# Performance work log

Hardware: AMD Instinct MI355X
Metric: run time of the kernel (lower is better)

The kernel has to match this reference:

```python
import jax, jax.numpy as jnp
import numpy as np
from jax import lax

DIM = 256
NUM_HEADS = 8
SPLIT = 7
IDX = 0  # vertical split: h_sp=h, w_sp=split_size
HEAD_DIM = DIM // NUM_HEADS
SCALE = HEAD_DIM ** -0.5


def setup_inputs() -> dict:
    key = jax.random.key(0)
    k1, k2, k3 = jax.random.split(key, 3)
    b, h, w = 16, 56, 56
    n = h * w
    qkv = jax.random.normal(k1, (3, b, n, DIM), dtype=jnp.float32)
    conv_w = jax.random.normal(k2, (DIM, 1, 3, 3), dtype=jnp.float32) * 0.1
    conv_b = jax.random.normal(k3, (DIM,), dtype=jnp.float32) * 0.1
    return {"qkv": qkv, "conv_w": conv_w, "conv_b": conv_b, "h": h, "w": w}


def _to_windows_heads(x, b, c, h, w, h_sp, w_sp):
    # (b, n, c) -> (b*nWin, num_heads, h_sp*w_sp, head_dim)
    x = x.transpose(0, 2, 1).reshape(b, c, h, w)
    x = x.reshape(b, c, h // h_sp, h_sp, w // w_sp, w_sp)
    x = x.transpose(0, 2, 4, 3, 5, 1).reshape(-1, h_sp * w_sp, c)
    return x.reshape(-1, h_sp * w_sp, NUM_HEADS, HEAD_DIM).transpose(0, 2, 1, 3)


def reference(qkv, conv_w, conv_b, h, w):
    q, k, v = qkv[0], qkv[1], qkv[2]
    b, n, c = q.shape
    h_sp, w_sp = (h, SPLIT) if IDX == 0 else (SPLIT, w)

    qw = _to_windows_heads(q, b, c, h, w, h_sp, w_sp) * SCALE
    kw = _to_windows_heads(k, b, c, h, w, h_sp, w_sp)

    # v as window images (b*nWin, c, h_sp, w_sp) for depthwise-conv LePE
    vimg = v.transpose(0, 2, 1).reshape(b, c, h, w)
    vimg = vimg.reshape(b, c, h // h_sp, h_sp, w // w_sp, w_sp)
    vimg = vimg.transpose(0, 2, 4, 1, 3, 5).reshape(-1, c, h_sp, w_sp)

    lepe = lax.conv_general_dilated(
        vimg, conv_w, window_strides=(1, 1), padding='SAME',
        dimension_numbers=('NCHW', 'OIHW', 'NCHW'), feature_group_count=c)
    lepe = lepe + conv_b[None, :, None, None]

    def _heads(t):  # (b', c, h_sp, w_sp) -> (b', heads, hw, head_dim)
        return t.reshape(-1, NUM_HEADS, HEAD_DIM, h_sp * w_sp).transpose(0, 1, 3, 2)

    vw = _heads(vimg)
    lepe = _heads(lepe)

    attn = jax.nn.softmax(jnp.einsum('whqd,whkd->whqk', qw, kw), axis=-1)
    x = jnp.einsum('whqk,whkd->whqd', attn, vw) + lepe  # (b', heads, hw, hd)

    x = x.transpose(0, 2, 1, 3).reshape(-1, h_sp * w_sp, c)
    # windows2img
    x = x.reshape(b, h // h_sp, w // w_sp, h_sp, w_sp, c)
    x = x.transpose(0, 1, 3, 2, 4, 5).reshape(b, h, w, c)
    return x.reshape(b, n, c)
```

## Files before the change

### kernel.cpp

```cpp
#include <hip/hip_runtime.h>
#include <math.h>


#define BATCH 16
#define HH 56
#define WW 56
#define WSP 7
#define NHEAD 8
#define HD 32
#define DIMC 256
#define NTOK 3136
#define S 392
#define SPAD 416
#define NCH 13
#define QT 25
#define QSCALE 0.17677669529663687f

typedef __attribute__((ext_vector_type(8))) short short8;
typedef __attribute__((ext_vector_type(4))) float f32x4;

#define MFMA(A, B, C) __builtin_amdgcn_mfma_f32_16x16x32_bf16((A), (B), (C), 0, 0, 0)

__device__ inline ushort bf16_rne(float f) {
    uint u = __float_as_uint(f);
    return (ushort)((u + 0x7FFFu + ((u >> 16) & 1u)) >> 16);
}
__device__ inline float bf16_f32(ushort h) { return __uint_as_float(((uint)h) << 16); }

__global__ __launch_bounds__(512, 1)
void lepe_attn_mfma(const float* __restrict__ qkv,
                    const float* __restrict__ conv_w,
                    const float* __restrict__ conv_b,
                    float* __restrict__ out)
{
    __shared__ ushort Kh_s[SPAD * HD];
    __shared__ ushort Kl_s[SPAD * HD];
    __shared__ ushort Vh_s[HD * SPAD];
    __shared__ ushort Vl_s[HD * SPAD];
    __shared__ ushort lepe_s[S * HD];
    __shared__ ushort P_s[8][2][16 * 40];

    const int tid  = threadIdx.x;
    const int lane = tid & 63;
    const int wv   = tid >> 6;
    const int ql   = lane & 15;
    const int g    = lane >> 4;
    const int slot = ((g ^ ((ql >> 1) & 3)) << 3);
    const int bid  = blockIdx.x;
    const int head = bid & 7;
    const int gw   = bid >> 3;
    const int b    = gw >> 3;
    const int wi   = gw & 7;
    const int coff = head * HD;

    const float* qbase = qkv + (size_t)b * NTOK * DIMC;
    const float* kbase = qkv + (size_t)(BATCH + b) * NTOK * DIMC;
    const float* vbase = qkv + (size_t)(2 * BATCH + b) * NTOK * DIMC;

    for (int j = tid; j < 32 * HD; j += 512) {
        const int d = j >> 5, o = j & 31;
        Vh_s[d * SPAD + 384 + o] = 0;
        Vl_s[d * SPAD + 384 + o] = 0;
    }

    for (int i = tid; i < S * 8; i += 512) {
        const int t  = i >> 3;
        const int f4 = i & 7;
        const int y  = t / WSP, x = t - y * WSP;
        const int n  = y * WW + wi * WSP + x;
        const float4 kk = *(const float4*)(kbase + (size_t)n * DIMC + coff + f4 * 4);
        const float4 vv = *(const float4*)(vbase + (size_t)n * DIMC + coff + f4 * 4);
        ushort h[4], l[4];
#pragma unroll
        for (int j = 0; j < 4; ++j) {
            const float kf = ((const float*)&kk)[j];
            h[j] = bf16_rne(kf);
            l[j] = bf16_rne(kf - bf16_f32(h[j]));
        }
        uint2 wh, wl;
        wh.x = (uint)h[0] | ((uint)h[1] << 16); wh.y = (uint)h[2] | ((uint)h[3] << 16);
        wl.x = (uint)l[0] | ((uint)l[1] << 16); wl.y = (uint)l[2] | ((uint)l[3] << 16);
        const int kidx = t * HD + ((f4 << 2) ^ (((t >> 1) & 3) << 3));
        *(uint2*)&Kh_s[kidx] = wh;
        *(uint2*)&Kl_s[kidx] = wl;
#pragma unroll
        for (int j = 0; j < 4; ++j) {
            const int d = f4 * 4 + j;
            const float vf = ((const float*)&vv)[j];
            const ushort vh = bf16_rne(vf);
            const int vidx = d * SPAD + (t ^ (((d >> 1) & 3) << 3));
            Vh_s[vidx] = vh;
            Vl_s[vidx] = bf16_rne(vf - bf16_f32(vh));
        }
    }
    __syncthreads();

    if (tid < 448) {
        const int d  = tid & 31;
        const int q  = tid >> 5;
        const int xl = q % 7;
        const int y0 = (q / 7) * 28;
        const int dsw = ((d >> 1) & 3) << 3;
        float wvv[9];
#pragma unroll
        for (int k = 0; k < 9; ++k) wvv[k] = conv_w[(coff + d) * 9 + k];
        const float bias = conv_b[coff + d];
        const ushort* vh = &Vh_s[d * SPAD];
        const ushort* vl = &Vl_s[d * SPAD];
        for (int y = y0; y < y0 + 28; ++y) {
            float acc = bias;
#pragma unroll
            for (int dy = -1; dy <= 1; ++dy) {
                const int yy = y + dy;
                if (yy < 0 || yy >= HH) continue;
#pragma unroll
                for (int dx = -1; dx <= 1; ++dx) {
                    const int xx = xl + dx;
                    if (xx < 0 || xx >= WSP) continue;
                    const int key = (yy * WSP + xx) ^ dsw;
                    acc = fmaf(wvv[(dy + 1) * 3 + (dx + 1)],
                               bf16_f32(vh[key]) + bf16_f32(vl[key]), acc);
                }
            }
            const int t = y * WSP + xl;
            lepe_s[t * HD + (d ^ ((t & 7) << 2))] = bf16_rne(acc);
        }
    }
    __syncthreads();

    ushort* Ph = &P_s[wv][0][0];
    ushort* Pl = &P_s[wv][1][0];

    for (int qt = wv; qt < QT; qt += 8) {
        const int qtok = qt * 16 + ql;
        const int qc   = (qtok < S) ? qtok : (S - 1);
        const int qy   = qc / WSP, qx = qc - qy * WSP;
        const float* qp = qbase + (size_t)(qy * WW + wi * WSP + qx) * DIMC + coff + g * 8;
        short8 Qh, Qlo;
#pragma unroll
        for (int j = 0; j < 8; ++j) {
            const float q = qp[j] * QSCALE;
            const ushort hh = bf16_rne(q);
            Qh[j]  = (short)hh;
            Qlo[j] = (short)bf16_rne(q - bf16_f32(hh));
        }
        f32x4 O0 = {0.f, 0.f, 0.f, 0.f};
        f32x4 O1 = {0.f, 0.f, 0.f, 0.f};
        float m = -INFINITY, lsum = 0.f;

        for (int c = 0; c < NCH; ++c) {
            const short8 KaH = *(const short8*)&Kh_s[(c * 32 + ql) * HD + slot];
            const short8 KaL = *(const short8*)&Kl_s[(c * 32 + ql) * HD + slot];
            const short8 KbH = *(const short8*)&Kh_s[(c * 32 + 16 + ql) * HD + slot];
            const short8 KbL = *(const short8*)&Kl_s[(c * 32 + 16 + ql) * HD + slot];
            f32x4 sa = {0.f, 0.f, 0.f, 0.f};
            f32x4 sb = {0.f, 0.f, 0.f, 0.f};
            sa = MFMA(KaH, Qh, sa); sa = MFMA(KaH, Qlo, sa); sa = MFMA(KaL, Qh, sa);
            sb = MFMA(KbH, Qh, sb); sb = MFMA(KbH, Qlo, sb); sb = MFMA(KbL, Qh, sb);

            if (c == NCH - 1) {
#pragma unroll
                for (int r = 0; r < 4; ++r) {
                    if (c * 32 + 4 * g + r >= S)      sa[r] = -1e30f;
                    if (c * 32 + 16 + 4 * g + r >= S) sb[r] = -1e30f;
                }
            }

            float tmax = fmaxf(fmaxf(fmaxf(sa[0], sa[1]), fmaxf(sa[2], sa[3])),
                               fmaxf(fmaxf(sb[0], sb[1]), fmaxf(sb[2], sb[3])));
            tmax = fmaxf(tmax, __shfl_xor(tmax, 16));
            tmax = fmaxf(tmax, __shfl_xor(tmax, 32));
            const float mnew = fmaxf(m, tmax);
            const float corr = __expf(m - mnew);
            m = mnew;
            lsum *= corr;
#pragma unroll
            for (int r = 0; r < 4; ++r) { O0[r] *= corr; O1[r] *= corr; }

            float pa[4], pb[4];
#pragma unroll
            for (int r = 0; r < 4; ++r) {
                pa[r] = __expf(sa[r] - m);
                pb[r] = __expf(sb[r] - m);
                lsum += pa[r] + pb[r];
            }
            ushort ah[4], al[4], bh[4], bl[4];
#pragma unroll
            for (int r = 0; r < 4; ++r) {
                ah[r] = bf16_rne(pa[r]); al[r] = bf16_rne(pa[r] - bf16_f32(ah[r]));
                bh[r] = bf16_rne(pb[r]); bl[r] = bf16_rne(pb[r] - bf16_f32(bh[r]));
            }
            uint2 w;
            w.x = (uint)ah[0] | ((uint)ah[1] << 16); w.y = (uint)ah[2] | ((uint)ah[3] << 16);
            *(uint2*)&Ph[ql * 40 + 4 * g] = w;
            w.x = (uint)bh[0] | ((uint)bh[1] << 16); w.y = (uint)bh[2] | ((uint)bh[3] << 16);
            *(uint2*)&Ph[ql * 40 + 16 + 4 * g] = w;
            w.x = (uint)al[0] | ((uint)al[1] << 16); w.y = (uint)al[2] | ((uint)al[3] << 16);
            *(uint2*)&Pl[ql * 40 + 4 * g] = w;
            w.x = (uint)bl[0] | ((uint)bl[1] << 16); w.y = (uint)bl[2] | ((uint)bl[3] << 16);
            *(uint2*)&Pl[ql * 40 + 16 + 4 * g] = w;

            const short8 PfH = *(const short8*)&Ph[ql * 40 + 8 * g];
            const short8 PfL = *(const short8*)&Pl[ql * 40 + 8 * g];
            const short8 V0H = *(const short8*)&Vh_s[ql * SPAD + c * 32 + slot];
            const short8 V0L = *(const short8*)&Vl_s[ql * SPAD + c * 32 + slot];
            const short8 V1H = *(const short8*)&Vh_s[(16 + ql) * SPAD + c * 32 + slot];
            const short8 V1L = *(const short8*)&Vl_s[(16 + ql) * SPAD + c * 32 + slot];
            O0 = MFMA(V0H, PfH, O0); O0 = MFMA(V0L, PfH, O0); O0 = MFMA(V0H, PfL, O0);
            O1 = MFMA(V1H, PfH, O1); O1 = MFMA(V1L, PfH, O1); O1 = MFMA(V1H, PfL, O1);
        }

        lsum += __shfl_xor(lsum, 16);
        lsum += __shfl_xor(lsum, 32);
        const float inv = 1.f / lsum;

        if (qtok < S) {
            const int oy = qtok / WSP, ox = qtok - oy * WSP;
            float* op = out + ((size_t)b * NTOK + oy * WW + wi * WSP + ox) * DIMC + coff;
            const uint2 w0 = *(const uint2*)&lepe_s[qtok * HD + ((g ^ (qtok & 7)) << 2)];
            const uint2 w1 = *(const uint2*)&lepe_s[qtok * HD + (((g + 4) ^ (qtok & 7)) << 2)];
            float4 o0v, o1v;
            o0v.x = O0[0] * inv + bf16_f32((ushort)(w0.x & 0xffff));
            o0v.y = O0[1] * inv + bf16_f32((ushort)(w0.x >> 16));
            o0v.z = O0[2] * inv + bf16_f32((ushort)(w0.y & 0xffff));
            o0v.w = O0[3] * inv + bf16_f32((ushort)(w0.y >> 16));
            o1v.x = O1[0] * inv + bf16_f32((ushort)(w1.x & 0xffff));
            o1v.y = O1[1] * inv + bf16_f32((ushort)(w1.x >> 16));
            o1v.z = O1[2] * inv + bf16_f32((ushort)(w1.y & 0xffff));
            o1v.w = O1[3] * inv + bf16_f32((ushort)(w1.y >> 16));
            *(float4*)(op + 4 * g)      = o0v;
            *(float4*)(op + 16 + 4 * g) = o1v;
        }
    }
}

extern "C" void kernel_launch(void* const* d_in, const int* in_sizes, int n_in,
                              void* d_out, int out_size, void* d_ws, size_t ws_size,
                              hipStream_t stream)
{
    const float* qkv    = (const float*)d_in[0];
    const float* conv_w = (const float*)d_in[1];
    const float* conv_b = (const float*)d_in[2];
    float* out = (float*)d_out;

    dim3 grid(BATCH * 8 * NHEAD);
    dim3 block(512);
    lepe_attn_mfma<<<grid, block, 0, stream>>>(qkv, conv_w, conv_b, out);
}
```

Baseline: 403.8 us.

## Switch split-bf16 MFMA attention to single fp16 MFMA and fuse LePE into epilogue

Replaces the three-MFMA bf16 hi/lo split emulation of fp32 with a single f16 MFMA per product for both QK and PV, halving K/V shared-memory footprint. The separate LePE conv phase, its shared buffer and one barrier are removed, and the depthwise conv is computed per query in the output epilogue from the fp16 V tile. It also adds a lazy softmax rescale that only runs when the max grows by more than 8, and raises launch bounds to allow more blocks per CU. Precision drops to fp16, which risks tolerance failures and overflow for large scores or values.

```diff
diff --git a/kernel.cpp b/kernel.cpp
--- a/kernel.cpp
+++ b/kernel.cpp
@@ -16,29 +16,23 @@
 #define QT 25
 #define QSCALE 0.17677669529663687f
 
-typedef __attribute__((ext_vector_type(8))) short short8;
+typedef __attribute__((ext_vector_type(8))) _Float16 half8;
+typedef __attribute__((ext_vector_type(4))) _Float16 half4;
 typedef __attribute__((ext_vector_type(4))) float f32x4;
 
-#define MFMA(A, B, C) __builtin_amdgcn_mfma_f32_16x16x32_bf16((A), (B), (C), 0, 0, 0)
-
-__device__ inline ushort bf16_rne(float f) {
-    uint u = __float_as_uint(f);
-    return (ushort)((u + 0x7FFFu + ((u >> 16) & 1u)) >> 16);
-}
-__device__ inline float bf16_f32(ushort h) { return __uint_as_float(((uint)h) << 16); }
-
-__global__ __launch_bounds__(512, 1)
-void lepe_attn_mfma(const float* __restrict__ qkv,
-                    const float* __restrict__ conv_w,
-                    const float* __restrict__ conv_b,
-                    float* __restrict__ out)
+#define MFMA(A, B, C) __builtin_amdgcn_mfma_f32_16x16x32_f16((A), (B), (C), 0, 0, 0)
+
+__global__ __launch_bounds__(512, 4)
+void lepe_attn_f16(const float* __restrict__ qkv,
+                   const float* __restrict__ conv_w,
+                   const float* __restrict__ conv_b,
+                   float* __restrict__ out)
 {
-    __shared__ ushort Kh_s[SPAD * HD];
-    __shared__ ushort Kl_s[SPAD * HD];
-    __shared__ ushort Vh_s[HD * SPAD];
-    __shared__ ushort Vl_s[HD * SPAD];
-    __shared__ ushort lepe_s[S * HD];
-    __shared__ ushort P_s[8][2][16 * 40];
+    __shared__ _Float16 K_s[SPAD * HD];
+    __shared__ _Float16 V_s[HD * SPAD];
+    __shared__ _Float16 P_s[8][16 * 40];
+    __shared__ float    cw_s[HD * 9];
+    __shared__ float    cb_s[HD];
 
     const int tid  = threadIdx.x;
     const int lane = tid & 63;
@@ -57,10 +51,13 @@
     const float* kbase = qkv + (size_t)(BATCH + b) * NTOK * DIMC;
     const float* vbase = qkv + (size_t)(2 * BATCH + b) * NTOK * DIMC;
 
-    for (int j = tid; j < 32 * HD; j += 512) {
-        const int d = j >> 5, o = j & 31;
-        Vh_s[d * SPAD + 384 + o] = 0;
-        Vl_s[d * SPAD + 384 + o] = 0;
+    for (int j = tid; j < HD * 9; j += 512) cw_s[j] = conv_w[coff * 9 + j];
+    if (tid < HD) cb_s[tid] = conv_b[coff + tid];
+
+    for (int j = tid; j < 768; j += 512) {
+        K_s[(392 + (j >> 5)) * HD + (j & 31)] = (_Float16)0.f;
+        const int d = j & 31, ko = j >> 5;
+        V_s[d * SPAD + ((392 + ko) ^ (((d >> 1) & 3) << 3))] = (_Float16)0.f;
     }
 
     for (int i = tid; i < S * 8; i += 512) {
@@ -70,93 +67,45 @@
         const int n  = y * WW + wi * WSP + x;
         const float4 kk = *(const float4*)(kbase + (size_t)n * DIMC + coff + f4 * 4);
         const float4 vv = *(const float4*)(vbase + (size_t)n * DIMC + coff + f4 * 4);
-        ushort h[4], l[4];
-#pragma unroll
-        for (int j = 0; j < 4; ++j) {
-            const float kf = ((const float*)&kk)[j];
-            h[j] = bf16_rne(kf);
-            l[j] = bf16_rne(kf - bf16_f32(h[j]));
-        }
-        uint2 wh, wl;
-        wh.x = (uint)h[0] | ((uint)h[1] << 16); wh.y = (uint)h[2] | ((uint)h[3] << 16);
-        wl.x = (uint)l[0] | ((uint)l[1] << 16); wl.y = (uint)l[2] | ((uint)l[3] << 16);
-        const int kidx = t * HD + ((f4 << 2) ^ (((t >> 1) & 3) << 3));
-        *(uint2*)&Kh_s[kidx] = wh;
-        *(uint2*)&Kl_s[kidx] = wl;
+        half4 kh;
+        kh[0] = (_Float16)kk.x; kh[1] = (_Float16)kk.y;
+        kh[2] = (_Float16)kk.z; kh[3] = (_Float16)kk.w;
+        *(half4*)&K_s[t * HD + ((f4 << 2) ^ (((t >> 1) & 3) << 3))] = kh;
 #pragma unroll
         for (int j = 0; j < 4; ++j) {
             const int d = f4 * 4 + j;
-            const float vf = ((const float*)&vv)[j];
-            const ushort vh = bf16_rne(vf);
-            const int vidx = d * SPAD + (t ^ (((d >> 1) & 3) << 3));
-            Vh_s[vidx] = vh;
-            Vl_s[vidx] = bf16_rne(vf - bf16_f32(vh));
+            V_s[d * SPAD + (t ^ (((d >> 1) & 3) << 3))] =
+                (_Float16)((const float*)&vv)[j];
         }
     }
     __syncthreads();
 
-    if (tid < 448) {
-        const int d  = tid & 31;
-        const int q  = tid >> 5;
-        const int xl = q % 7;
-        const int y0 = (q / 7) * 28;
-        const int dsw = ((d >> 1) & 3) << 3;
-        float wvv[9];
-#pragma unroll
-        for (int k = 0; k < 9; ++k) wvv[k] = conv_w[(coff + d) * 9 + k];
-        const float bias = conv_b[coff + d];
-        const ushort* vh = &Vh_s[d * SPAD];
-        const ushort* vl = &Vl_s[d * SPAD];
-        for (int y = y0; y < y0 + 28; ++y) {
-            float acc = bias;
-#pragma unroll
-            for (int dy = -1; dy <= 1; ++dy) {
-                const int yy = y + dy;
-                if (yy < 0 || yy >= HH) continue;
-#pragma unroll
-                for (int dx = -1; dx <= 1; ++dx) {
-                    const int xx = xl + dx;
-                    if (xx < 0 || xx >= WSP) continue;
-                    const int key = (yy * WSP + xx) ^ dsw;
-                    acc = fmaf(wvv[(dy + 1) * 3 + (dx + 1)],
-                               bf16_f32(vh[key]) + bf16_f32(vl[key]), acc);
-                }
-            }
-            const int t = y * WSP + xl;
-            lepe_s[t * HD + (d ^ ((t & 7) << 2))] = bf16_rne(acc);
-        }
-    }
-    __syncthreads();
-
-    ushort* Ph = &P_s[wv][0][0];
-    ushort* Pl = &P_s[wv][1][0];
+    _Float16* Ph = &P_s[wv][0];
 
     for (int qt = wv; qt < QT; qt += 8) {
         const int qtok = qt * 16 + ql;
         const int qc   = (qtok < S) ? qtok : (S - 1);
         const int qy   = qc / WSP, qx = qc - qy * WSP;
         const float* qp = qbase + (size_t)(qy * WW + wi * WSP + qx) * DIMC + coff + g * 8;
-        short8 Qh, Qlo;
-#pragma unroll
-        for (int j = 0; j < 8; ++j) {
-            const float q = qp[j] * QSCALE;
-            const ushort hh = bf16_rne(q);
-            Qh[j]  = (short)hh;
-            Qlo[j] = (short)bf16_rne(q - bf16_f32(hh));
-        }
+        const float4 qa = *(const float4*)qp;
+        const float4 qb = *(const float4*)(qp + 4);
+        half8 Qf;
+        Qf[0] = (_Float16)(qa.x * QSCALE); Qf[1] = (_Float16)(qa.y * QSCALE);
+        Qf[2] = (_Float16)(qa.z * QSCALE); Qf[3] = (_Float16)(qa.w * QSCALE);
+        Qf[4] = (_Float16)(qb.x * QSCALE); Qf[5] = (_Float16)(qb.y * QSCALE);
+        Qf[6] = (_Float16)(qb.z * QSCALE); Qf[7] = (_Float16)(qb.w * QSCALE);
+
         f32x4 O0 = {0.f, 0.f, 0.f, 0.f};
         f32x4 O1 = {0.f, 0.f, 0.f, 0.f};
         float m = -INFINITY, lsum = 0.f;
 
         for (int c = 0; c < NCH; ++c) {
-            const short8 KaH = *(const short8*)&Kh_s[(c * 32 + ql) * HD + slot];
-            const short8 KaL = *(const short8*)&Kl_s[(c * 32 + ql) * HD + slot];
-            const short8 KbH = *(const short8*)&Kh_s[(c * 32 + 16 + ql) * HD + slot];
-            const short8 KbL = *(const short8*)&Kl_s[(c * 32 + 16 + ql) * HD + slot];
+            const half8 Ka = *(const half8*)&K_s[(c * 32 + ql) * HD + slot];
+            const half8 Kb = *(const half8*)&K_s[(c * 32 + 16 + ql) * HD + slot];
             f32x4 sa = {0.f, 0.f, 0.f, 0.f};
             f32x4 sb = {0.f, 0.f, 0.f, 0.f};
-            sa = MFMA(KaH, Qh, sa); sa = MFMA(KaH, Qlo, sa); sa = MFMA(KaL, Qh, sa);
-            sb = MFMA(KbH, Qh, sb); sb = MFMA(KbH, Qlo, sb); sb = MFMA(KbL, Qh, sb);
+            sa = MFMA(Ka, Qf, sa);
+            sb = MFMA(Kb, Qf, sb);
 
             if (c == NCH - 1) {
 #pragma unroll
@@ -170,44 +119,39 @@
                                fmaxf(fmaxf(sb[0], sb[1]), fmaxf(sb[2], sb[3])));
             tmax = fmaxf(tmax, __shfl_xor(tmax, 16));
             tmax = fmaxf(tmax, __shfl_xor(tmax, 32));
-            const float mnew = fmaxf(m, tmax);
-            const float corr = __expf(m - mnew);
-            m = mnew;
-            lsum *= corr;
-#pragma unroll
-            for (int r = 0; r < 4; ++r) { O0[r] *= corr; O1[r] *= corr; }
+
+            if (!__all(tmax - m <= 8.0f)) {
+                const float mnew = fmaxf(m, tmax);
+                const float corr = __expf(m - mnew);
+                m = mnew;
+                lsum *= corr;
+#pragma unroll
+                for (int r = 0; r < 4; ++r) { O0[r] *= corr; O1[r] *= corr; }
+            }
 
             float pa[4], pb[4];
 #pragma unroll
             for (int r = 0; r < 4; ++r) {
                 pa[r] = __expf(sa[r] - m);
                 pb[r] = __expf(sb[r] - m);
-                lsum += pa[r] + pb[r];
-            }
-            ushort ah[4], al[4], bh[4], bl[4];
+            }
+            lsum += ((pa[0] + pa[1]) + (pa[2] + pa[3])) +
+                    ((pb[0] + pb[1]) + (pb[2] + pb[3]));
+
+            half4 wa, wb;
 #pragma unroll
             for (int r = 0; r < 4; ++r) {
-                ah[r] = bf16_rne(pa[r]); al[r] = bf16_rne(pa[r] - bf16_f32(ah[r]));
-                bh[r] = bf16_rne(pb[r]); bl[r] = bf16_rne(pb[r] - bf16_f32(bh[r]));
-            }
-            uint2 w;
-            w.x = (uint)ah[0] | ((uint)ah[1] << 16); w.y = (uint)ah[2] | ((uint)ah[3] << 16);
-            *(uint2*)&Ph[ql * 40 + 4 * g] = w;
-            w.x = (uint)bh[0] | ((uint)bh[1] << 16); w.y = (uint)bh[2] | ((uint)bh[3] << 16);
-            *(uint2*)&Ph[ql * 40 + 16 + 4 * g] = w;
-            w.x = (uint)al[0] | ((uint)al[1] << 16); w.y = (uint)al[2] | ((uint)al[3] << 16);
-            *(uint2*)&Pl[ql * 40 + 4 * g] = w;
-            w.x = (uint)bl[0] | ((uint)bl[1] << 16); w.y = (uint)bl[2] | ((uint)bl[3] << 16);
-            *(uint2*)&Pl[ql * 40 + 16 + 4 * g] = w;
-
-            const short8 PfH = *(const short8*)&Ph[ql * 40 + 8 * g];
-            const short8 PfL = *(const short8*)&Pl[ql * 40 + 8 * g];
-            const short8 V0H = *(const short8*)&Vh_s[ql * SPAD + c * 32 + slot];
-            const short8 V0L = *(const short8*)&Vl_s[ql * SPAD + c * 32 + slot];
-            const short8 V1H = *(const short8*)&Vh_s[(16 + ql) * SPAD + c * 32 + slot];
-            const short8 V1L = *(const short8*)&Vl_s[(16 + ql) * SPAD + c * 32 + slot];
-            O0 = MFMA(V0H, PfH, O0); O0 = MFMA(V0L, PfH, O0); O0 = MFMA(V0H, PfL, O0);
-            O1 = MFMA(V1H, PfH, O1); O1 = MFMA(V1L, PfH, O1); O1 = MFMA(V1H, PfL, O1);
+                wa[r] = (_Float16)pa[r];
+                wb[r] = (_Float16)pb[r];
+            }
+            *(half4*)&Ph[ql * 40 + 4 * g]      = wa;
+            *(half4*)&Ph[ql * 40 + 16 + 4 * g] = wb;
+
+            const half8 Pf = *(const half8*)&Ph[ql * 40 + 8 * g];
+            const half8 V0 = *(const half8*)&V_s[ql * SPAD + c * 32 + slot];
+            const half8 V1 = *(const half8*)&V_s[(16 + ql) * SPAD + c * 32 + slot];
+            O0 = MFMA(V0, Pf, O0);
+            O1 = MFMA(V1, Pf, O1);
         }
 
         lsum += __shfl_xor(lsum, 16);
@@ -215,19 +159,36 @@
         const float inv = 1.f / lsum;
 
         if (qtok < S) {
-            const int oy = qtok / WSP, ox = qtok - oy * WSP;
-            float* op = out + ((size_t)b * NTOK + oy * WW + wi * WSP + ox) * DIMC + coff;
-            const uint2 w0 = *(const uint2*)&lepe_s[qtok * HD + ((g ^ (qtok & 7)) << 2)];
-            const uint2 w1 = *(const uint2*)&lepe_s[qtok * HD + (((g + 4) ^ (qtok & 7)) << 2)];
+            float lp[8];
+#pragma unroll
+            for (int jj = 0; jj < 4; ++jj) {
+                lp[jj]     = cb_s[4 * g + jj];
+                lp[4 + jj] = cb_s[16 + 4 * g + jj];
+            }
+#pragma unroll
+            for (int dy = -1; dy <= 1; ++dy) {
+                const int yy = qy + dy;
+                if (yy < 0 || yy >= HH) continue;
+#pragma unroll
+                for (int dx = -1; dx <= 1; ++dx) {
+                    const int xx = qx + dx;
+                    if (xx < 0 || xx >= WSP) continue;
+                    const int t  = yy * WSP + xx;
+                    const int kt = (dy + 1) * 3 + (dx + 1);
+#pragma unroll
+                    for (int jj = 0; jj < 8; ++jj) {
+                        const int d = (jj < 4) ? (4 * g + jj) : (16 + 4 * g + (jj - 4));
+                        lp[jj] += cw_s[d * 9 + kt] *
+                                  (float)V_s[d * SPAD + (t ^ (((d >> 1) & 3) << 3))];
+                    }
+                }
+            }
+            float* op = out + ((size_t)b * NTOK + qy * WW + wi * WSP + qx) * DIMC + coff;
             float4 o0v, o1v;
-            o0v.x = O0[0] * inv + bf16_f32((ushort)(w0.x & 0xffff));
-            o0v.y = O0[1] * inv + bf16_f32((ushort)(w0.x >> 16));
-            o0v.z = O0[2] * inv + bf16_f32((ushort)(w0.y & 0xffff));
-            o0v.w = O0[3] * inv + bf16_f32((ushort)(w0.y >> 16));
-            o1v.x = O1[0] * inv + bf16_f32((ushort)(w1.x & 0xffff));
-            o1v.y = O1[1] * inv + bf16_f32((ushort)(w1.x >> 16));
-            o1v.z = O1[2] * inv + bf16_f32((ushort)(w1.y & 0xffff));
-            o1v.w = O1[3] * inv + bf16_f32((ushort)(w1.y >> 16));
+            o0v.x = O0[0] * inv + lp[0]; o0v.y = O0[1] * inv + lp[1];
+            o0v.z = O0[2] * inv + lp[2]; o0v.w = O0[3] * inv + lp[3];
+            o1v.x = O1[0] * inv + lp[4]; o1v.y = O1[1] * inv + lp[5];
+            o1v.z = O1[2] * inv + lp[6]; o1v.w = O1[3] * inv + lp[7];
             *(float4*)(op + 4 * g)      = o0v;
             *(float4*)(op + 16 + 4 * g) = o1v;
         }
@@ -245,5 +206,5 @@
 
     dim3 grid(BATCH * 8 * NHEAD);
     dim3 block(512);
-    lepe_attn_mfma<<<grid, block, 0, stream>>>(qkv, conv_w, conv_b, out);
+    lepe_attn_f16<<<grid, block, 0, stream>>>(qkv, conv_w, conv_b, out);
 }
```

Result: slower. 438.2 us (+8.5%).
